# Kernel tuning notes

Measured on AMD Instinct MI355X. Metric: run time of the kernel, lower is better.

The kernel has to match this reference:

```python
import jax, jax.numpy as jnp
import numpy as np

N_RULE, N_TOKEN = 256, 32000
F_IN, F_ACT, H = 512, 512, 1024  # input_feature_size, action_feature_size, output_feature_size
L, B = 128, 64


def setup_inputs() -> dict:
    key = jax.random.key(0)
    ks = jax.random.split(key, 8)
    s_ih = 1.0 / np.sqrt(H)
    return {
        "input_feature": jax.random.normal(ks[0], (B, F_IN), dtype=jnp.float32),
        "previous_actions": jax.random.randint(ks[1], (L, B, 3), 0, N_RULE, dtype=jnp.int64),
        "mask": jnp.ones((L, B), dtype=jnp.float32),
        "hidden_state": jnp.zeros((B, H), dtype=jnp.float32),
        "state": jnp.zeros((B, H), dtype=jnp.float32),
        "rule_embed": jax.random.normal(ks[2], (N_RULE, F_ACT), dtype=jnp.float32),
        "token_embed": jax.random.normal(ks[3], (N_TOKEN, F_ACT), dtype=jnp.float32),
        "W_ih": jax.random.uniform(ks[4], (4 * H, F_IN + F_ACT), jnp.float32, -s_ih, s_ih),
        "W_hh": jax.random.uniform(ks[5], (4 * H, H), jnp.float32, -s_ih, s_ih),
        "b_ih": jax.random.uniform(ks[6], (4 * H,), jnp.float32, -s_ih, s_ih),
        "b_hh": jax.random.uniform(ks[7], (4 * H,), jnp.float32, -s_ih, s_ih),
    }


def _masked_embed(table, idx):
    # EmbeddingWithMask: index == -1 maps to the zero vector
    valid = (idx != -1)
    emb = table[jnp.where(valid, idx, 0)]
    return emb * valid[..., None].astype(table.dtype)


def reference(input_feature, previous_actions, mask, hidden_state, state,
              rule_embed, token_embed, W_ih, W_hh, b_ih, b_hh):
    prev_rules = previous_actions[..., 0]   # (L, B)
    prev_tokens = previous_actions[..., 1]  # (L, B)
    act = _masked_embed(rule_embed, prev_rules) + _masked_embed(token_embed, prev_tokens)  # (L,B,F_ACT)

    # Per-step input is concat([input_feature, act_t]); precompute the whole
    # input projection x @ W_ih^T + biases once (big batched GEMM).
    l, b = act.shape[0], act.shape[1]
    Wx, Wa = W_ih[:, :input_feature.shape[1]], W_ih[:, input_feature.shape[1]:]
    xg = (input_feature @ Wx.T)[None] + jnp.einsum('lba,ga->lbg', act, Wa) + (b_ih + b_hh)  # (L,B,4H)

    def step(carry, xg_t):
        h, c = carry
        g = xg_t + h @ W_hh.T                     # (B, 4H)
        i, f, gg, o = jnp.split(g, 4, axis=-1)    # torch LSTMCell gate order
        i, f, o = jax.nn.sigmoid(i), jax.nn.sigmoid(f), jax.nn.sigmoid(o)
        c1 = f * c + i * jnp.tanh(gg)
        h1 = o * jnp.tanh(c1)
        return (h1, c1), h1

    (h_n, c_n), hs = jax.lax.scan(step, (hidden_state, state), xg)
    return hs, h_n, c_n
```

## Files before the change

### kernel.cpp

```cpp
#include <hip/hip_runtime.h>
#include <hip/hip_bf16.h>

typedef __attribute__((ext_vector_type(8))) short bf16x8;
typedef __attribute__((ext_vector_type(4))) float f32x4;

#define L_SEQ 128
#define BATCH 64
#define HID   1024
#define GATES 4096
#define NWG   64
#define UPW   16
#define FSTR  16

__device__ inline short f2bf_s(float f) {
  __hip_bfloat16 h = __float2bfloat16(f);
  union { __hip_bfloat16 hh; short s; } u; u.hh = h; return u.s;
}
__device__ inline float bf2f_u(unsigned short s) {
  union { unsigned u; float f; } u; u.u = ((unsigned)s) << 16; return u.f;
}
__device__ inline float sigm(float x) { return 1.f / (1.f + __expf(-x)); }
__device__ inline float tanh_f(float x) {
  x = fminf(x, 15.f);
  float e = __expf(2.f * x);
  return (e - 1.f) / (e + 1.f);
}

__global__ void k_init(const float* __restrict__ hidden, const float* __restrict__ x,
                       const float* __restrict__ bih, const float* __restrict__ bhh,
                       __hip_bfloat16* __restrict__ h_all0, __hip_bfloat16* __restrict__ x_bf,
                       float* __restrict__ bias2, unsigned* __restrict__ bar) {
  int gid = blockIdx.x * 256 + threadIdx.x;
  if (gid < BATCH * HID) h_all0[gid] = __float2bfloat16(hidden[gid]);
  if (gid < BATCH * 512) x_bf[gid]  = __float2bfloat16(x[gid]);
  if (gid < GATES)       bias2[gid] = bih[gid] + bhh[gid];
  if (gid < 16384)       bar[gid] = 0u;
}

__global__ void k_wsplit(const float* __restrict__ Wih,
                         __hip_bfloat16* __restrict__ Wx, __hip_bfloat16* __restrict__ Wa) {
  int e = blockIdx.x * 256 + threadIdx.x;
  int g = e >> 7;
  int ko = (e & 127) << 3;
  const float* src = Wih + (size_t)g * 1024 + ko;
  float4 f0 = *(const float4*)(src);
  float4 f1 = *(const float4*)(src + 4);
  union { bf16x8 v; short s[8]; } o;
  o.s[0]=f2bf_s(f0.x); o.s[1]=f2bf_s(f0.y); o.s[2]=f2bf_s(f0.z); o.s[3]=f2bf_s(f0.w);
  o.s[4]=f2bf_s(f1.x); o.s[5]=f2bf_s(f1.y); o.s[6]=f2bf_s(f1.z); o.s[7]=f2bf_s(f1.w);
  if (ko < 512) *(bf16x8*)(Wx + (size_t)g * 512 + ko)        = o.v;
  else          *(bf16x8*)(Wa + (size_t)g * 512 + (ko - 512)) = o.v;
}

__global__ void k_act(const int* __restrict__ pa, const float* __restrict__ remb,
                      const float* __restrict__ temb, __hip_bfloat16* __restrict__ act) {
  int row = blockIdx.x;
  int tid = threadIdx.x;
  int r  = pa[row * 3 + 0];
  int tk = pa[row * 3 + 1];
  float sr = (r  != -1) ? 1.f : 0.f; int ri = (r  != -1) ? r  : 0;
  float st = (tk != -1) ? 1.f : 0.f; int ti = (tk != -1) ? tk : 0;
  const float4* rr = (const float4*)(remb + (size_t)ri * 512);
  const float4* tr = (const float4*)(temb + (size_t)ti * 512);
  float4 a = rr[tid * 2], b4 = rr[tid * 2 + 1];
  float4 c4 = tr[tid * 2], d4 = tr[tid * 2 + 1];
  union { bf16x8 v; short s[8]; } o;
  o.s[0]=f2bf_s(sr*a.x + st*c4.x);  o.s[1]=f2bf_s(sr*a.y + st*c4.y);
  o.s[2]=f2bf_s(sr*a.z + st*c4.z);  o.s[3]=f2bf_s(sr*a.w + st*c4.w);
  o.s[4]=f2bf_s(sr*b4.x + st*d4.x); o.s[5]=f2bf_s(sr*b4.y + st*d4.y);
  o.s[6]=f2bf_s(sr*b4.z + st*d4.z); o.s[7]=f2bf_s(sr*b4.w + st*d4.w);
  *(bf16x8*)(act + (size_t)row * 512 + tid * 8) = o.v;
}

template<int MODE>
__global__ __launch_bounds__(256) void k_gemm(
    const __hip_bfloat16* __restrict__ A, const __hip_bfloat16* __restrict__ B,
    const float* __restrict__ addend, float* __restrict__ Cf,
    __hip_bfloat16* __restrict__ Cb, int M) {
  __shared__ __hip_bfloat16 At[128][72];
  __shared__ __hip_bfloat16 Bt[128][72];
  const int tid = threadIdx.x;
  const int m0 = blockIdx.y * 128, n0 = blockIdx.x * 128;
  const int w = tid >> 6, lane = tid & 63;
  const int wm = (w >> 1) * 64, wn = (w & 1) * 64;
  const int lm = lane & 15, quad = lane >> 4;
  const int srow = tid >> 1, shalf = (tid & 1) * 32;
  f32x4 acc[4][4] = {};
  for (int k0 = 0; k0 < 512; k0 += 64) {
    int arow = m0 + srow;
    if (MODE == 0 && arow >= M) arow = M - 1;
    const bf16x8* ag = (const bf16x8*)(A + (size_t)arow * 512 + k0 + shalf);
    const bf16x8* bg = (const bf16x8*)(B + (size_t)(n0 + srow) * 512 + k0 + shalf);
    bf16x8 av[4], bv[4];
#pragma unroll
    for (int q = 0; q < 4; ++q) { av[q] = ag[q]; bv[q] = bg[q]; }
    __syncthreads();
#pragma unroll
    for (int q = 0; q < 4; ++q) {
      *(bf16x8*)(&At[srow][shalf + q * 8]) = av[q];
      *(bf16x8*)(&Bt[srow][shalf + q * 8]) = bv[q];
    }
    __syncthreads();
#pragma unroll
    for (int ks = 0; ks < 2; ++ks) {
      bf16x8 af[4], bf[4];
#pragma unroll
      for (int i = 0; i < 4; ++i) {
        af[i] = *(const bf16x8*)(&At[wm + i * 16 + lm][ks * 32 + quad * 8]);
        bf[i] = *(const bf16x8*)(&Bt[wn + i * 16 + lm][ks * 32 + quad * 8]);
      }
#pragma unroll
      for (int i = 0; i < 4; ++i)
#pragma unroll
        for (int j = 0; j < 4; ++j)
          acc[i][j] = __builtin_amdgcn_mfma_f32_16x16x32_bf16(af[i], bf[j], acc[i][j], 0, 0, 0);
    }
  }
#pragma unroll
  for (int i = 0; i < 4; ++i) {
    int mrow = m0 + wm + i * 16 + quad * 4;
#pragma unroll
    for (int j = 0; j < 4; ++j) {
      int ncol = n0 + wn + j * 16 + lm;
#pragma unroll
      for (int r = 0; r < 4; ++r) {
        int m = mrow + r;
        if (MODE == 0) {
          if (m < M) Cf[(size_t)m * GATES + ncol] = acc[i][j][r] + addend[ncol];
        } else {
          float v = acc[i][j][r] + addend[(size_t)(m & 63) * GATES + ncol];
          Cb[(size_t)m * GATES + ncol] = __float2bfloat16(v);
        }
      }
    }
  }
}

__global__ __launch_bounds__(256, 1) void k_scan(
    const float* __restrict__ Whh, const __hip_bfloat16* __restrict__ xg,
    const float* __restrict__ state_in, __hip_bfloat16* __restrict__ h_all,
    float* __restrict__ out_hs, float* __restrict__ out_hn, float* __restrict__ out_cn,
    unsigned* __restrict__ bar) {
  __shared__ __hip_bfloat16 Wl[64 * 1032];
  __shared__ float gl[64 * 68];
  __shared__ unsigned sdep;
  const int tid = threadIdx.x;
  const int wg = blockIdx.x;
  const int u0 = wg * UPW;
  for (int e = tid; e < 64 * 128; e += 256) {
    int j = e >> 7;
    int ko = (e & 127) << 3;
    int gate = j >> 4, uu = j & 15;
    const float* src = Whh + (size_t)(gate * HID + u0 + uu) * HID + ko;
    float4 f0 = *(const float4*)(src);
    float4 f1 = *(const float4*)(src + 4);
    union { bf16x8 v; short s[8]; } o;
    o.s[0]=f2bf_s(f0.x); o.s[1]=f2bf_s(f0.y); o.s[2]=f2bf_s(f0.z); o.s[3]=f2bf_s(f0.w);
    o.s[4]=f2bf_s(f1.x); o.s[5]=f2bf_s(f1.y); o.s[6]=f2bf_s(f1.z); o.s[7]=f2bf_s(f1.w);
    *(bf16x8*)(&Wl[j * 1032 + ko]) = o.v;
  }
  const int b = tid >> 2, x = tid & 3;
  f32x4 c4i = *(const f32x4*)(state_in + (size_t)b * HID + u0 + x * 4);
  float cc[4] = {c4i[0], c4i[1], c4i[2], c4i[3]};
  const int w = tid >> 6, lane = tid & 63;
  const int lm = lane & 15, quad = lane >> 4;
  const int m0 = w * 16;
  unsigned* flags = bar;
  if (tid == 0) sdep = 0;
  union U64 { unsigned long long u; unsigned short s[4]; };
  U64 xv[4];
  {
    const unsigned short* xp = (const unsigned short*)xg + (size_t)b * GATES + u0 + x * 4;
#pragma unroll
    for (int g = 0; g < 4; ++g) xv[g].u = *(const unsigned long long*)(xp + g * 1024);
  }
  unsigned dep = 0;
  __syncthreads();
  for (int t = 0; t < L_SEQ; ++t) {
    const __hip_bfloat16* hsrc = h_all + ((size_t)t + dep) * (BATCH * HID);
    const bf16x8* arow = (const bf16x8*)(hsrc + (m0 + lm) * HID + quad * 8);
    bf16x8 areg[32];
#pragma unroll
    for (int kq = 0; kq < 32; ++kq) areg[kq] = arow[kq * 4];
    __builtin_amdgcn_sched_barrier(0);
    f32x4 acc[4] = {{0.f, 0.f, 0.f, 0.f}, {0.f, 0.f, 0.f, 0.f},
                    {0.f, 0.f, 0.f, 0.f}, {0.f, 0.f, 0.f, 0.f}};
#pragma unroll
    for (int kq = 0; kq < 32; ++kq) {
#pragma unroll
      for (int n = 0; n < 4; ++n) {
        bf16x8 bfrag = *(const bf16x8*)(&Wl[(n * 16 + lm) * 1032 + kq * 32 + quad * 8]);
        acc[n] = __builtin_amdgcn_mfma_f32_16x16x32_bf16(areg[kq], bfrag, acc[n], 0, 0, 0);
      }
    }
#pragma unroll
    for (int n = 0; n < 4; ++n)
#pragma unroll
      for (int r = 0; r < 4; ++r)
        gl[(m0 + quad * 4 + r) * 68 + n * 16 + lm] = acc[n][r];
    __syncthreads();
    f32x4 gi4 = *(const f32x4*)(&gl[b * 68 + 0  + x * 4]);
    f32x4 gf4 = *(const f32x4*)(&gl[b * 68 + 16 + x * 4]);
    f32x4 gg4 = *(const f32x4*)(&gl[b * 68 + 32 + x * 4]);
    f32x4 go4 = *(const f32x4*)(&gl[b * 68 + 48 + x * 4]);
    float hv[4];
    U64 hp;
#pragma unroll
    for (int j = 0; j < 4; ++j) {
      float ii = sigm(gi4[j] + bf2f_u(xv[0].s[j]));
      float ff = sigm(gf4[j] + bf2f_u(xv[1].s[j]));
      float gv = tanh_f(gg4[j] + bf2f_u(xv[2].s[j]));
      float oo = sigm(go4[j] + bf2f_u(xv[3].s[j]));
      cc[j] = ff * cc[j] + ii * gv;
      hv[j] = oo * tanh_f(cc[j]);
      hp.s[j] = (unsigned short)f2bf_s(hv[j]);
    }
    f32x4 hv4 = {hv[0], hv[1], hv[2], hv[3]};
    float* hsout = out_hs + ((size_t)t * BATCH + b) * HID + u0 + x * 4;
    if (t == L_SEQ - 1) {
      __builtin_nontemporal_store(hv4, (f32x4*)hsout);
      f32x4 cc4 = {cc[0], cc[1], cc[2], cc[3]};
      __builtin_nontemporal_store(hv4, (f32x4*)(out_hn + (size_t)b * HID + u0 + x * 4));
      __builtin_nontemporal_store(cc4, (f32x4*)(out_cn + (size_t)b * HID + u0 + x * 4));
    } else {
      unsigned long long* hdst =
          (unsigned long long*)(h_all + ((size_t)(t + 1)) * (BATCH * HID));
      __hip_atomic_store(&hdst[(((size_t)b * HID + u0) >> 2) + x], hp.u,
                         __ATOMIC_RELAXED, __HIP_MEMORY_SCOPE_SYSTEM);
      unsigned target = (unsigned)(t + 1);
      __builtin_amdgcn_s_waitcnt(0);
      if (tid == 0)
        __hip_atomic_store(&flags[wg * FSTR], target, __ATOMIC_RELAXED,
                           __HIP_MEMORY_SCOPE_SYSTEM);
      __builtin_amdgcn_sched_barrier(0);
      __builtin_nontemporal_store(hv4, (f32x4*)hsout);
      {
        const unsigned short* xp = (const unsigned short*)xg +
            ((size_t)(t + 1) * BATCH + b) * GATES + u0 + x * 4;
#pragma unroll
        for (int g = 0; g < 4; ++g) xv[g].u = *(const unsigned long long*)(xp + g * 1024);
      }
      if (tid < NWG) {
        bool ok = false;
        unsigned long long bl;
        for (;;) {
          if (!ok) {
            unsigned v = __hip_atomic_load(&flags[tid * FSTR], __ATOMIC_RELAXED,
                                           __HIP_MEMORY_SCOPE_SYSTEM);
            ok = (v >= target);
          }
          bl = __ballot(ok);
          if (bl == 0xFFFFFFFFFFFFFFFFull) break;
          __builtin_amdgcn_s_sleep(1);
        }
        if (tid == 0) sdep = (unsigned)((bl >> 44) >> 20);
      }
      __syncthreads();
      dep = sdep;
    }
  }
}

extern "C" void kernel_launch(void* const* d_in, const int* in_sizes, int n_in,
                              void* d_out, int out_size, void* d_ws, size_t ws_size,
                              hipStream_t stream) {
  const float* x      = (const float*)d_in[0];
  const int*   pa     = (const int*)d_in[1];
  const float* hidden = (const float*)d_in[3];
  const float* state  = (const float*)d_in[4];
  const float* remb   = (const float*)d_in[5];
  const float* temb   = (const float*)d_in[6];
  const float* Wih    = (const float*)d_in[7];
  const float* Whh    = (const float*)d_in[8];
  const float* bih    = (const float*)d_in[9];
  const float* bhh    = (const float*)d_in[10];

  char* ws = (char*)d_ws;
  size_t off = 0;
  auto take = [&](size_t bytes) { char* p = ws + off; off += (bytes + 255) & ~(size_t)255; return p; };
  unsigned* bar         = (unsigned*)take(16384 * 4);
  __hip_bfloat16* h_all = (__hip_bfloat16*)take((size_t)L_SEQ * BATCH * HID * 2);
  __hip_bfloat16* x_bf  = (__hip_bfloat16*)take((size_t)BATCH * 512 * 2);
  float* bias2          = (float*)take((size_t)GATES * 4);
  __hip_bfloat16* Wx    = (__hip_bfloat16*)take((size_t)GATES * 512 * 2);
  __hip_bfloat16* Wa    = (__hip_bfloat16*)take((size_t)GATES * 512 * 2);
  __hip_bfloat16* act   = (__hip_bfloat16*)take((size_t)8192 * 512 * 2);
  float* y0             = (float*)take((size_t)BATCH * GATES * 4);
  __hip_bfloat16* xg    = (__hip_bfloat16*)take((size_t)8192 * GATES * 2);

  float* out_hs = (float*)d_out;
  float* out_hn = out_hs + (size_t)L_SEQ * BATCH * HID;
  float* out_cn = out_hn + (size_t)BATCH * HID;

  hipLaunchKernelGGL(k_init, dim3(256), dim3(256), 0, stream, hidden, x, bih, bhh, h_all, x_bf, bias2, bar);
  hipLaunchKernelGGL(k_wsplit, dim3(2048), dim3(256), 0, stream, Wih, Wx, Wa);
  hipLaunchKernelGGL(k_act, dim3(8192), dim3(64), 0, stream, pa, remb, temb, act);
  hipLaunchKernelGGL((k_gemm<0>), dim3(32, 1), dim3(256), 0, stream,
                     x_bf, Wx, bias2, y0, (__hip_bfloat16*)nullptr, 64);
  hipLaunchKernelGGL((k_gemm<1>), dim3(32, 64), dim3(256), 0, stream,
                     act, Wa, y0, (float*)nullptr, xg, 8192);
  void* args[] = { (void*)&Whh, (void*)&xg, (void*)&state, (void*)&h_all,
                   (void*)&out_hs, (void*)&out_hn, (void*)&out_cn, (void*)&bar };
  (void)hipLaunchCooperativeKernel((void*)k_scan, dim3(NWG), dim3(256), args, 0, stream);
}
```

Measured before the change: 1.158 ms.

## Replace flag barrier with sentinel-value polling on hidden-state data

Removes the per-step global flag barrier across the 64 workgroups. Each consumer now polls the h-state slots directly, spinning on a canary NaN pattern that is pre-written into every future slot by the init kernel. The h buffer and the LDS weight layout are reorganized into 32-wide k-chunks so that a producer's slice is contiguous. The scan is also launched as a normal kernel instead of a cooperative one. This cuts barrier latency and lets a workgroup start its MFMAs on chunks that have already arrived. In exchange, the init kernel must fill the whole buffer with canaries, it relies on 8-byte atomicity, and a bounded spin could silently read stale data.

```diff
diff --git a/kernel.cpp b/kernel.cpp
--- a/kernel.cpp
+++ b/kernel.cpp
@@ -10,7 +10,9 @@
 #define GATES 4096
 #define NWG   64
 #define UPW   16
-#define FSTR  16
+#define SLOTB (BATCH * HID * 2)
+#define CAN32 0x7FC17FC1u
+#define CAN64 0x7FC17FC17FC17FC1ull
 
 __device__ inline short f2bf_s(float f) {
   __hip_bfloat16 h = __float2bfloat16(f);
@@ -25,16 +27,29 @@
   float e = __expf(2.f * x);
   return (e - 1.f) / (e + 1.f);
 }
+__device__ inline bool is_can(unsigned long long q) {
+  return ((unsigned)q == CAN32) | ((unsigned)(q >> 32) == CAN32);
+}
 
 __global__ void k_init(const float* __restrict__ hidden, const float* __restrict__ x,
                        const float* __restrict__ bih, const float* __restrict__ bhh,
                        __hip_bfloat16* __restrict__ h_all0, __hip_bfloat16* __restrict__ x_bf,
-                       float* __restrict__ bias2, unsigned* __restrict__ bar) {
+                       float* __restrict__ bias2) {
   int gid = blockIdx.x * 256 + threadIdx.x;
-  if (gid < BATCH * HID) h_all0[gid] = __float2bfloat16(hidden[gid]);
+  unsigned long long* hw = (unsigned long long*)h_all0;
+  if (gid < BATCH * HID / 4) {
+    int c = gid >> 8, wi = gid & 255, b = wi >> 2, xq = wi & 3;
+    float4 f = *(const float4*)(hidden + (size_t)b * HID + c * 16 + xq * 4);
+    union { unsigned long long u; unsigned short s[4]; } p;
+    p.s[0] = (unsigned short)f2bf_s(f.x); p.s[1] = (unsigned short)f2bf_s(f.y);
+    p.s[2] = (unsigned short)f2bf_s(f.z); p.s[3] = (unsigned short)f2bf_s(f.w);
+    __hip_atomic_store(&hw[gid], p.u, __ATOMIC_RELAXED, __HIP_MEMORY_SCOPE_SYSTEM);
+  }
   if (gid < BATCH * 512) x_bf[gid]  = __float2bfloat16(x[gid]);
   if (gid < GATES)       bias2[gid] = bih[gid] + bhh[gid];
-  if (gid < 16384)       bar[gid] = 0u;
+  unsigned long long* cw = hw + (size_t)BATCH * HID / 4;
+  for (size_t i = gid; i < (size_t)L_SEQ * BATCH * HID / 4; i += 65536)
+    __hip_atomic_store(&cw[i], CAN64, __ATOMIC_RELAXED, __HIP_MEMORY_SCOPE_SYSTEM);
 }
 
 __global__ void k_wsplit(const float* __restrict__ Wih,
@@ -139,11 +154,9 @@
 __global__ __launch_bounds__(256, 1) void k_scan(
     const float* __restrict__ Whh, const __hip_bfloat16* __restrict__ xg,
     const float* __restrict__ state_in, __hip_bfloat16* __restrict__ h_all,
-    float* __restrict__ out_hs, float* __restrict__ out_hn, float* __restrict__ out_cn,
-    unsigned* __restrict__ bar) {
-  __shared__ __hip_bfloat16 Wl[64 * 1032];
+    float* __restrict__ out_hs, float* __restrict__ out_hn, float* __restrict__ out_cn) {
+  __shared__ __hip_bfloat16 Wl[32 * 2048];
   __shared__ float gl[64 * 68];
-  __shared__ unsigned sdep;
   const int tid = threadIdx.x;
   const int wg = blockIdx.x;
   const int u0 = wg * UPW;
@@ -157,7 +170,7 @@
     union { bf16x8 v; short s[8]; } o;
     o.s[0]=f2bf_s(f0.x); o.s[1]=f2bf_s(f0.y); o.s[2]=f2bf_s(f0.z); o.s[3]=f2bf_s(f0.w);
     o.s[4]=f2bf_s(f1.x); o.s[5]=f2bf_s(f1.y); o.s[6]=f2bf_s(f1.z); o.s[7]=f2bf_s(f1.w);
-    *(bf16x8*)(&Wl[j * 1032 + ko]) = o.v;
+    *(bf16x8*)(&Wl[(ko >> 5) * 2048 + j * 32 + ((ko >> 3) & 3) * 8]) = o.v;
   }
   const int b = tid >> 2, x = tid & 3;
   f32x4 c4i = *(const f32x4*)(state_in + (size_t)b * HID + u0 + x * 4);
@@ -165,8 +178,6 @@
   const int w = tid >> 6, lane = tid & 63;
   const int lm = lane & 15, quad = lane >> 4;
   const int m0 = w * 16;
-  unsigned* flags = bar;
-  if (tid == 0) sdep = 0;
   union U64 { unsigned long long u; unsigned short s[4]; };
   U64 xv[4];
   {
@@ -174,23 +185,43 @@
 #pragma unroll
     for (int g = 0; g < 4; ++g) xv[g].u = *(const unsigned long long*)(xp + g * 1024);
   }
-  unsigned dep = 0;
+  int budget = 1 << 20;
   __syncthreads();
   for (int t = 0; t < L_SEQ; ++t) {
-    const __hip_bfloat16* hsrc = h_all + ((size_t)t + dep) * (BATCH * HID);
-    const bf16x8* arow = (const bf16x8*)(hsrc + (m0 + lm) * HID + quad * 8);
-    bf16x8 areg[32];
-#pragma unroll
-    for (int kq = 0; kq < 32; ++kq) areg[kq] = arow[kq * 4];
+    const char* a0 = (const char*)h_all + (size_t)t * SLOTB
+                   + (size_t)(quad >> 1) * 2048 + (size_t)(m0 + lm) * 32
+                   + (size_t)(quad & 1) * 16;
+    union BF8 { bf16x8 v; unsigned long long q[2]; } areg[32];
+#pragma unroll
+    for (int kq = 0; kq < 32; ++kq) {
+      areg[kq].q[0] = __hip_atomic_load(
+          (const unsigned long long*)(a0 + (size_t)kq * 4096),
+          __ATOMIC_RELAXED, __HIP_MEMORY_SCOPE_SYSTEM);
+      areg[kq].q[1] = __hip_atomic_load(
+          (const unsigned long long*)(a0 + (size_t)kq * 4096 + 8),
+          __ATOMIC_RELAXED, __HIP_MEMORY_SCOPE_SYSTEM);
+    }
     __builtin_amdgcn_sched_barrier(0);
-    f32x4 acc[4] = {{0.f, 0.f, 0.f, 0.f}, {0.f, 0.f, 0.f, 0.f},
-                    {0.f, 0.f, 0.f, 0.f}, {0.f, 0.f, 0.f, 0.f}};
+    f32x4 acc[4] = {{0.f,0.f,0.f,0.f}, {0.f,0.f,0.f,0.f},
+                    {0.f,0.f,0.f,0.f}, {0.f,0.f,0.f,0.f}};
 #pragma unroll
     for (int kq = 0; kq < 32; ++kq) {
+      if (t > 0) {
+        while (__any(is_can(areg[kq].q[0]) || is_can(areg[kq].q[1]))) {
+          if (--budget < 0) break;
+          __builtin_amdgcn_s_sleep(1);
+          areg[kq].q[0] = __hip_atomic_load(
+              (const unsigned long long*)(a0 + (size_t)kq * 4096),
+              __ATOMIC_RELAXED, __HIP_MEMORY_SCOPE_SYSTEM);
+          areg[kq].q[1] = __hip_atomic_load(
+              (const unsigned long long*)(a0 + (size_t)kq * 4096 + 8),
+              __ATOMIC_RELAXED, __HIP_MEMORY_SCOPE_SYSTEM);
+        }
+      }
 #pragma unroll
       for (int n = 0; n < 4; ++n) {
-        bf16x8 bfrag = *(const bf16x8*)(&Wl[(n * 16 + lm) * 1032 + kq * 32 + quad * 8]);
-        acc[n] = __builtin_amdgcn_mfma_f32_16x16x32_bf16(areg[kq], bfrag, acc[n], 0, 0, 0);
+        bf16x8 bfrag = *(const bf16x8*)(&Wl[kq * 2048 + (n * 16 + lm) * 32 + quad * 8]);
+        acc[n] = __builtin_amdgcn_mfma_f32_16x16x32_bf16(areg[kq].v, bfrag, acc[n], 0, 0, 0);
       }
     }
 #pragma unroll
@@ -223,16 +254,9 @@
       __builtin_nontemporal_store(hv4, (f32x4*)(out_hn + (size_t)b * HID + u0 + x * 4));
       __builtin_nontemporal_store(cc4, (f32x4*)(out_cn + (size_t)b * HID + u0 + x * 4));
     } else {
-      unsigned long long* hdst =
-          (unsigned long long*)(h_all + ((size_t)(t + 1)) * (BATCH * HID));
-      __hip_atomic_store(&hdst[(((size_t)b * HID + u0) >> 2) + x], hp.u,
-                         __ATOMIC_RELAXED, __HIP_MEMORY_SCOPE_SYSTEM);
-      unsigned target = (unsigned)(t + 1);
-      __builtin_amdgcn_s_waitcnt(0);
-      if (tid == 0)
-        __hip_atomic_store(&flags[wg * FSTR], target, __ATOMIC_RELAXED,
-                           __HIP_MEMORY_SCOPE_SYSTEM);
-      __builtin_amdgcn_sched_barrier(0);
+      unsigned long long* hdst = (unsigned long long*)
+          ((char*)h_all + (size_t)(t + 1) * SLOTB + (size_t)wg * 2048 + (size_t)b * 32);
+      __hip_atomic_store(&hdst[x], hp.u, __ATOMIC_RELAXED, __HIP_MEMORY_SCOPE_SYSTEM);
       __builtin_nontemporal_store(hv4, (f32x4*)hsout);
       {
         const unsigned short* xp = (const unsigned short*)xg +
@@ -240,23 +264,7 @@
 #pragma unroll
         for (int g = 0; g < 4; ++g) xv[g].u = *(const unsigned long long*)(xp + g * 1024);
       }
-      if (tid < NWG) {
-        bool ok = false;
-        unsigned long long bl;
-        for (;;) {
-          if (!ok) {
-            unsigned v = __hip_atomic_load(&flags[tid * FSTR], __ATOMIC_RELAXED,
-                                           __HIP_MEMORY_SCOPE_SYSTEM);
-            ok = (v >= target);
-          }
-          bl = __ballot(ok);
-          if (bl == 0xFFFFFFFFFFFFFFFFull) break;
-          __builtin_amdgcn_s_sleep(1);
-        }
-        if (tid == 0) sdep = (unsigned)((bl >> 44) >> 20);
-      }
       __syncthreads();
-      dep = sdep;
     }
   }
 }
@@ -278,8 +286,7 @@
   char* ws = (char*)d_ws;
   size_t off = 0;
   auto take = [&](size_t bytes) { char* p = ws + off; off += (bytes + 255) & ~(size_t)255; return p; };
-  unsigned* bar         = (unsigned*)take(16384 * 4);
-  __hip_bfloat16* h_all = (__hip_bfloat16*)take((size_t)L_SEQ * BATCH * HID * 2);
+  __hip_bfloat16* h_all = (__hip_bfloat16*)take((size_t)(L_SEQ + 1) * BATCH * HID * 2);
   __hip_bfloat16* x_bf  = (__hip_bfloat16*)take((size_t)BATCH * 512 * 2);
   float* bias2          = (float*)take((size_t)GATES * 4);
   __hip_bfloat16* Wx    = (__hip_bfloat16*)take((size_t)GATES * 512 * 2);
@@ -292,14 +299,13 @@
   float* out_hn = out_hs + (size_t)L_SEQ * BATCH * HID;
   float* out_cn = out_hn + (size_t)BATCH * HID;
 
-  hipLaunchKernelGGL(k_init, dim3(256), dim3(256), 0, stream, hidden, x, bih, bhh, h_all, x_bf, bias2, bar);
+  hipLaunchKernelGGL(k_init, dim3(256), dim3(256), 0, stream, hidden, x, bih, bhh, h_all, x_bf, bias2);
   hipLaunchKernelGGL(k_wsplit, dim3(2048), dim3(256), 0, stream, Wih, Wx, Wa);
   hipLaunchKernelGGL(k_act, dim3(8192), dim3(64), 0, stream, pa, remb, temb, act);
   hipLaunchKernelGGL((k_gemm<0>), dim3(32, 1), dim3(256), 0, stream,
                      x_bf, Wx, bias2, y0, (__hip_bfloat16*)nullptr, 64);
   hipLaunchKernelGGL((k_gemm<1>), dim3(32, 64), dim3(256), 0, stream,
                      act, Wa, y0, (float*)nullptr, xg, 8192);
-  void* args[] = { (void*)&Whh, (void*)&xg, (void*)&state, (void*)&h_all,
-                   (void*)&out_hs, (void*)&out_hn, (void*)&out_cn, (void*)&bar };
-  (void)hipLaunchCooperativeKernel((void*)k_scan, dim3(NWG), dim3(256), args, 0, stream);
-}
+  hipLaunchKernelGGL(k_scan, dim3(NWG), dim3(256), 0, stream,
+                     Whh, xg, state, h_all, out_hs, out_hn, out_cn);
+}
```

After: 1.827 ms. 1.58x slower.
